# Kernel optimization log

Measured on AMD Instinct MI355X. Metric: run time of the kernel, lower is better.

The kernel has to match this reference:

```python
import jax, jax.numpy as jnp
import numpy as np

D_MODEL = 512
DK = 4
DV = 8
HIDD = 10
HEAD = D_MODEL // DV  # 64
LN_EPS = 1e-5


def setup_inputs() -> dict:
    key = jax.random.key(0)
    ks = jax.random.split(key, 10)
    B, S, Se = 8, 512, 512
    u = jax.random.uniform  # torch.rand initializer for attention weights
    n = jax.random.normal
    return {
        "x": n(ks[0], (B, S, D_MODEL), jnp.float32),
        "x_enc": n(ks[1], (B, Se, D_MODEL), jnp.float32),
        "WqM": u(ks[2], (D_MODEL, HEAD * DK), jnp.float32),
        "WkM": u(ks[3], (D_MODEL, HEAD * DK), jnp.float32),
        "WvM": u(ks[4], (D_MODEL, HEAD * DV), jnp.float32),
        "ln_g": jnp.ones((D_MODEL,), jnp.float32),
        "ln_b": jnp.zeros((D_MODEL,), jnp.float32),
        "fc1_w": n(ks[5], (HIDD, D_MODEL), jnp.float32) * (1.0 / np.sqrt(D_MODEL)),
        "fc1_b": jnp.zeros((HIDD,), jnp.float32),
        "fc2_w": n(ks[6], (D_MODEL, HIDD), jnp.float32) * (1.0 / np.sqrt(HIDD)),
        "fc2_b": jnp.zeros((D_MODEL,), jnp.float32),
    }


def _attention(Xq, Xkv, WqM, WkM, WvM, causal_mul_mask):
    # NOTE: cross-attention in the source also uses WqM/WkM/WvM (Wq/Wk/Wv unused).
    B, Sq, _ = Xq.shape
    Sk = Xkv.shape[1]
    Q = (Xq @ WqM).reshape(B, Sq, HEAD, DK)
    K = (Xkv @ WkM).reshape(B, Sk, HEAD, DK)
    V = (Xkv @ WvM).reshape(B, Sk, HEAD, DV)
    score = jnp.einsum('bqhd,bkhd->bhqk', Q, K) / np.sqrt(DK).astype(np.float32)
    if causal_mul_mask:
        # Faithful quirk: multiplicative tril mask on scores (NOT additive -inf).
        score = score * jnp.tril(jnp.ones((Sq, Sk), score.dtype))
    w = jax.nn.softmax(score, axis=-1)
    out = jnp.einsum('bhqk,bkhd->bqhd', w, V)
    return out.reshape(B, Sq, HEAD * DV)  # HEAD*DV == d_model


def _layernorm(x, g, b):
    mu = jnp.mean(x, axis=-1, keepdims=True)
    var = jnp.mean(jnp.square(x - mu), axis=-1, keepdims=True)
    return (x - mu) * jax.lax.rsqrt(var + LN_EPS) * g + b


def reference(x, x_enc, WqM, WkM, WvM, ln_g, ln_b, fc1_w, fc1_b, fc2_w, fc2_b):
    fx = _attention(x, x, WqM, WkM, WvM, causal_mul_mask=True)
    fx = _attention(fx, x_enc, WqM, WkM, WvM, causal_mul_mask=False)
    y = _layernorm(x + fx, ln_g, ln_b)
    h = jax.nn.relu(y @ fc1_w.T + fc1_b)
    return h @ fc2_w.T + fc2_b
```

## Files before the change

kernel.cpp:

```cpp
#include <hip/hip_runtime.h>
#include <math.h>

#define D_MODEL 512
#define BATCH 8
#define SEQ 512
#define HEAD 64
#define DK 4
#define DV 8
#define HIDD 10

#define MR 32
#define KC 32
#define NC 256

__global__ __launch_bounds__(256) void proj_kernel(
    const float* __restrict__ xq, const float* __restrict__ xkv,
    const float* __restrict__ Wq, const float* __restrict__ Wk,
    const float* __restrict__ Wv,
    float* __restrict__ Q2, float* __restrict__ K2, float* __restrict__ V2)
{
    __shared__ float xt[KC * MR];
    __shared__ float wt[KC * NC];

    const int t  = threadIdx.x;
    const int bj = blockIdx.x & 3;
    const int br = blockIdx.x >> 2;
    const int r0 = br * MR;

    const float* X; const float* W; int ldw; int c0;
    if (bj == 0)      { X = xq;  W = Wq; ldw = 256; c0 = 0;   }
    else if (bj == 1) { X = xkv; W = Wk; ldw = 256; c0 = 0;   }
    else if (bj == 2) { X = xkv; W = Wv; ldw = 512; c0 = 0;   }
    else              { X = xkv; W = Wv; ldw = 512; c0 = 256; }

    const int rg = t >> 6;
    const int cq = t & 63;
    const int rs = t & 31;
    const int kq = t >> 5;

    float4 acc[8];
#pragma unroll
    for (int r = 0; r < 8; ++r) acc[r] = make_float4(0.f, 0.f, 0.f, 0.f);

    for (int kc = 0; kc < D_MODEL; kc += KC) {
        const float4 xa = *(const float4*)(X + (long)(r0 + rs) * D_MODEL + kc + kq * 4);
        xt[(kq * 4 + 0) * MR + rs] = xa.x;
        xt[(kq * 4 + 1) * MR + rs] = xa.y;
        xt[(kq * 4 + 2) * MR + rs] = xa.z;
        xt[(kq * 4 + 3) * MR + rs] = xa.w;

#pragma unroll
        for (int i = 0; i < 8; ++i) {
            const int row = i * 4 + rg;
            *(float4*)(wt + row * NC + cq * 4) =
                *(const float4*)(W + (long)(kc + row) * ldw + c0 + cq * 4);
        }
        __syncthreads();

#pragma unroll 4
        for (int k = 0; k < KC; ++k) {
            const float4 w4 = *(const float4*)(wt + k * NC + cq * 4);
            const float4 x0 = *(const float4*)(xt + k * MR + rg * 8);
            const float4 x1 = *(const float4*)(xt + k * MR + rg * 8 + 4);
            const float xr[8] = {x0.x, x0.y, x0.z, x0.w, x1.x, x1.y, x1.z, x1.w};
#pragma unroll
            for (int r = 0; r < 8; ++r) {
                acc[r].x = fmaf(xr[r], w4.x, acc[r].x);
                acc[r].y = fmaf(xr[r], w4.y, acc[r].y);
                acc[r].z = fmaf(xr[r], w4.z, acc[r].z);
                acc[r].w = fmaf(xr[r], w4.w, acc[r].w);
            }
        }
        __syncthreads();
    }

    const int b = r0 >> 9;
    const int sb = (r0 & 511) + rg * 8;
    if (bj <= 1) {
        float* dst = (bj == 0) ? Q2 : K2;
#pragma unroll
        for (int r = 0; r < 8; ++r)
            *(float4*)(dst + (((long)b * HEAD + cq) * SEQ + sb + r) * 4) = acc[r];
    } else {
        const int col = c0 + cq * 4;
        const int h = col >> 3;
        const int off = col & 7;
#pragma unroll
        for (int r = 0; r < 8; ++r)
            *(float4*)(V2 + (((long)b * HEAD + h) * SEQ + sb + r) * 8 + off) = acc[r];
    }
}

__global__ __launch_bounds__(256) void attn_kernel(
    const float* __restrict__ Q2, const float* __restrict__ K2,
    const float* __restrict__ V2, float* __restrict__ O, int causal)
{
    extern __shared__ float smem[];
    float* Kl = smem;
    float* Vl = smem + SEQ * DK;
    float* cs = Vl + SEQ * DV;

    const int t = threadIdx.x;
    const int bh = blockIdx.x >> 1;
    const int qhalf = blockIdx.x & 1;
    const int b = bh >> 6;
    const int h = bh & 63;

    const float4* Ks = (const float4*)(K2 + (long)bh * SEQ * DK);
    ((float4*)Kl)[t]       = Ks[t];
    ((float4*)Kl)[t + 256] = Ks[t + 256];
    const float4* Vs = (const float4*)(V2 + (long)bh * SEQ * DV);
#pragma unroll
    for (int i = 0; i < 4; ++i)
        ((float4*)Vl)[t + i * 256] = Vs[t + i * 256];
    __syncthreads();

    if (causal) {
        const int ch = t >> 3, d = t & 7;
        float s16 = 0.f;
#pragma unroll
        for (int i = 0; i < 16; ++i) s16 += Vl[(ch * 16 + i) * 8 + d];
        cs[ch * 8 + d] = s16;
        __syncthreads();
        if (t < 8) {
            cs[256 + t] = 0.f;
            float run = 0.f;
            for (int c2 = 31; c2 >= 0; --c2) {
                run += cs[c2 * 8 + t];
                cs[c2 * 8 + t] = run;
            }
        }
        __syncthreads();
    }

    const int q = qhalf * 256 + t;
    const float4 qv = *(const float4*)(Q2 + ((long)bh * SEQ + q) * 4);
    const float q0 = qv.x * 0.5f, q1 = qv.y * 0.5f;
    const float q2 = qv.z * 0.5f, q3 = qv.w * 0.5f;

    const int bound = causal ? q : (SEQ - 1);

    float m = -INFINITY, l = 0.f;
    float a0=0.f,a1=0.f,a2=0.f,a3=0.f,a4=0.f,a5=0.f,a6=0.f,a7=0.f;

    int s0 = 0;
    for (; s0 + 8 <= bound + 1; s0 += 8) {
        float sc[8];
#pragma unroll
        for (int i = 0; i < 8; ++i) {
            const float4 k4 = *(const float4*)(Kl + (s0 + i) * 4);
            sc[i] = fmaf(q0, k4.x, fmaf(q1, k4.y, fmaf(q2, k4.z, q3 * k4.w)));
        }
        float gm = fmaxf(fmaxf(fmaxf(sc[0], sc[1]), fmaxf(sc[2], sc[3])),
                         fmaxf(fmaxf(sc[4], sc[5]), fmaxf(sc[6], sc[7])));
        if (gm > m) {
            float scale = __expf(m - gm);
            l *= scale;
            a0*=scale; a1*=scale; a2*=scale; a3*=scale;
            a4*=scale; a5*=scale; a6*=scale; a7*=scale;
            m = gm;
        }
#pragma unroll
        for (int i = 0; i < 8; ++i) {
            float p = __expf(sc[i] - m);
            l += p;
            const float4 v0 = *(const float4*)(Vl + (s0 + i) * 8);
            const float4 v1 = *(const float4*)(Vl + (s0 + i) * 8 + 4);
            a0 = fmaf(p, v0.x, a0); a1 = fmaf(p, v0.y, a1);
            a2 = fmaf(p, v0.z, a2); a3 = fmaf(p, v0.w, a3);
            a4 = fmaf(p, v1.x, a4); a5 = fmaf(p, v1.y, a5);
            a6 = fmaf(p, v1.z, a6); a7 = fmaf(p, v1.w, a7);
        }
    }
    for (int s = s0; s <= bound; ++s) {
        const float4 k4 = *(const float4*)(Kl + s * 4);
        float sc = fmaf(q0, k4.x, fmaf(q1, k4.y, fmaf(q2, k4.z, q3 * k4.w)));
        if (sc > m) {
            float scale = __expf(m - sc);
            l *= scale;
            a0*=scale; a1*=scale; a2*=scale; a3*=scale;
            a4*=scale; a5*=scale; a6*=scale; a7*=scale;
            m = sc;
        }
        float p = __expf(sc - m);
        l += p;
        const float4 v0 = *(const float4*)(Vl + s * 8);
        const float4 v1 = *(const float4*)(Vl + s * 8 + 4);
        a0 = fmaf(p, v0.x, a0); a1 = fmaf(p, v0.y, a1);
        a2 = fmaf(p, v0.z, a2); a3 = fmaf(p, v0.w, a3);
        a4 = fmaf(p, v1.x, a4); a5 = fmaf(p, v1.y, a5);
        a6 = fmaf(p, v1.z, a6); a7 = fmaf(p, v1.w, a7);
    }

    if (causal && q < SEQ - 1) {
        float M = fmaxf(m, 0.f);
        float scale = __expf(m - M);
        float pm = __expf(-M);
        l = l * scale + pm * (float)(SEQ - 1 - q);
        int nq = q + 1;
        int cq2 = nq >> 4;
        float sv[8];
#pragma unroll
        for (int d = 0; d < 8; ++d) sv[d] = cs[(cq2 + 1) * 8 + d];
        for (int s = nq; s < (cq2 + 1) * 16; ++s) {
            const float4 v0 = *(const float4*)(Vl + s * 8);
            const float4 v1 = *(const float4*)(Vl + s * 8 + 4);
            sv[0]+=v0.x; sv[1]+=v0.y; sv[2]+=v0.z; sv[3]+=v0.w;
            sv[4]+=v1.x; sv[5]+=v1.y; sv[6]+=v1.z; sv[7]+=v1.w;
        }
        a0 = a0*scale + pm*sv[0]; a1 = a1*scale + pm*sv[1];
        a2 = a2*scale + pm*sv[2]; a3 = a3*scale + pm*sv[3];
        a4 = a4*scale + pm*sv[4]; a5 = a5*scale + pm*sv[5];
        a6 = a6*scale + pm*sv[6]; a7 = a7*scale + pm*sv[7];
    }

    float inv = 1.0f / l;
    const long obase = (long)b * SEQ * 512 + (long)q * 512 + h * DV;
    *(float4*)(O + obase)     = make_float4(a0*inv, a1*inv, a2*inv, a3*inv);
    *(float4*)(O + obase + 4) = make_float4(a4*inv, a5*inv, a6*inv, a7*inv);
}

__global__ __launch_bounds__(256) void ln_mlp_kernel(
    const float* __restrict__ x, const float* __restrict__ fx,
    const float* __restrict__ g, const float* __restrict__ beta,
    const float* __restrict__ w1, const float* __restrict__ b1,
    const float* __restrict__ w2, const float* __restrict__ b2,
    float* __restrict__ out)
{
    const int t = threadIdx.x;
    const int lane = t & 63;
    const int row = blockIdx.x * 4 + (t >> 6);
    const long base = (long)row * D_MODEL;
    const int e0 = lane * 8;

    const float4 xa = *(const float4*)(x + base + e0);
    const float4 xb = *(const float4*)(x + base + e0 + 4);
    const float4 fa = *(const float4*)(fx + base + e0);
    const float4 fb = *(const float4*)(fx + base + e0 + 4);
    float z[8] = {xa.x+fa.x, xa.y+fa.y, xa.z+fa.z, xa.w+fa.w,
                  xb.x+fb.x, xb.y+fb.y, xb.z+fb.z, xb.w+fb.w};

    float sum = 0.f;
#pragma unroll
    for (int j = 0; j < 8; ++j) sum += z[j];
#pragma unroll
    for (int o = 32; o > 0; o >>= 1) sum += __shfl_xor(sum, o);
    float mu = sum * (1.0f / 512.0f);

    float d[8], ss = 0.f;
#pragma unroll
    for (int j = 0; j < 8; ++j) { d[j] = z[j] - mu; ss += d[j] * d[j]; }
#pragma unroll
    for (int o = 32; o > 0; o >>= 1) ss += __shfl_xor(ss, o);
    float rs = rsqrtf(ss * (1.0f / 512.0f) + 1e-5f);

    const float4 ga = *(const float4*)(g + e0);
    const float4 gb = *(const float4*)(g + e0 + 4);
    const float4 ba = *(const float4*)(beta + e0);
    const float4 bb = *(const float4*)(beta + e0 + 4);
    const float gg[8] = {ga.x,ga.y,ga.z,ga.w,gb.x,gb.y,gb.z,gb.w};
    const float bt[8] = {ba.x,ba.y,ba.z,ba.w,bb.x,bb.y,bb.z,bb.w};
    float y[8];
#pragma unroll
    for (int j = 0; j < 8; ++j) y[j] = d[j] * rs * gg[j] + bt[j];

    float part[HIDD];
#pragma unroll
    for (int i = 0; i < HIDD; ++i) {
        const float4 wa = *(const float4*)(w1 + i * 512 + e0);
        const float4 wb = *(const float4*)(w1 + i * 512 + e0 + 4);
        part[i] = y[0]*wa.x + y[1]*wa.y + y[2]*wa.z + y[3]*wa.w
                + y[4]*wb.x + y[5]*wb.y + y[6]*wb.z + y[7]*wb.w;
    }
#pragma unroll
    for (int i = 0; i < HIDD; ++i)
#pragma unroll
        for (int o = 32; o > 0; o >>= 1) part[i] += __shfl_xor(part[i], o);

    float hv[HIDD];
#pragma unroll
    for (int i = 0; i < HIDD; ++i) hv[i] = fmaxf(part[i] + b1[i], 0.f);

    float o8[8];
#pragma unroll
    for (int j = 0; j < 8; ++j) o8[j] = b2[e0 + j];
#pragma unroll
    for (int i = 0; i < HIDD; ++i)
#pragma unroll
        for (int j = 0; j < 8; ++j)
            o8[j] = fmaf(hv[i], w2[(long)(e0 + j) * 10 + i], o8[j]);

    *(float4*)(out + base + e0)     = make_float4(o8[0], o8[1], o8[2], o8[3]);
    *(float4*)(out + base + e0 + 4) = make_float4(o8[4], o8[5], o8[6], o8[7]);
}

extern "C" void kernel_launch(void* const* d_in, const int* in_sizes, int n_in,
                              void* d_out, int out_size, void* d_ws, size_t ws_size,
                              hipStream_t stream) {
    (void)in_sizes; (void)n_in; (void)out_size; (void)ws_size;
    const float* x    = (const float*)d_in[0];
    const float* xenc = (const float*)d_in[1];
    const float* Wq   = (const float*)d_in[2];
    const float* Wk   = (const float*)d_in[3];
    const float* Wv   = (const float*)d_in[4];
    const float* ln_g = (const float*)d_in[5];
    const float* ln_b = (const float*)d_in[6];
    const float* w1   = (const float*)d_in[7];
    const float* b1   = (const float*)d_in[8];
    const float* w2   = (const float*)d_in[9];
    const float* b2   = (const float*)d_in[10];
    float* out = (float*)d_out;

    float* ws = (float*)d_ws;
    float* Q2 = ws;
    float* K2 = Q2 + 1048576;
    float* V2 = K2 + 1048576;
    float* A  = V2 + 2097152;

    const int nrows = BATCH * SEQ;
    const size_t lds_cross  = (size_t)(SEQ * DK + SEQ * DV) * 4;
    const size_t lds_causal = lds_cross + (size_t)(33 * DV) * 4;
    const int proj_grid = (nrows / MR) * 4;

    proj_kernel<<<dim3(proj_grid), 256, 0, stream>>>(x, x, Wq, Wk, Wv, Q2, K2, V2);
    attn_kernel<<<dim3(BATCH * HEAD * 2), 256, lds_causal, stream>>>(Q2, K2, V2, A, 1);

    proj_kernel<<<dim3(proj_grid), 256, 0, stream>>>(A, xenc, Wq, Wk, Wv, Q2, K2, V2);
    attn_kernel<<<dim3(BATCH * HEAD * 2), 256, lds_cross, stream>>>(Q2, K2, V2, A, 0);

    ln_mlp_kernel<<<dim3(nrows / 4), 256, 0, stream>>>(x, A, ln_g, ln_b,
                                                       w1, b1, w2, b2, out);
}
```

Measured before the change: 341.9 us.

## Hoist cross-attention K/V projection into first proj pass, split-K Q projection

The first projection kernel now also computes the cross-attention K and V from x_enc, giving 7 column-block jobs in one launch instead of recomputing them later. The second projection shrinks to a dedicated Q-only kernel that splits K into two halves with small tiles, writing two partial Q buffers that the attention kernel sums on load. Softmax exponentials switch to exp2 with log2(e) folded into the query scale. The aim is better GPU fill for the small Q projection and less work on the serial path, at the cost of more workspace and an extra Q read in attention.

```diff
diff --git a/kernel.cpp b/kernel.cpp
--- a/kernel.cpp
+++ b/kernel.cpp
@@ -13,25 +13,37 @@
 #define KC 32
 #define NC 256
 
+__device__ __forceinline__ float4 fma4(float s, float4 w, float4 a) {
+    a.x = fmaf(s, w.x, a.x); a.y = fmaf(s, w.y, a.y);
+    a.z = fmaf(s, w.z, a.z); a.w = fmaf(s, w.w, a.w);
+    return a;
+}
+
 __global__ __launch_bounds__(256) void proj_kernel(
-    const float* __restrict__ xq, const float* __restrict__ xkv,
+    const float* __restrict__ x, const float* __restrict__ xe,
     const float* __restrict__ Wq, const float* __restrict__ Wk,
     const float* __restrict__ Wv,
-    float* __restrict__ Q2, float* __restrict__ K2, float* __restrict__ V2)
+    float* __restrict__ Q2, float* __restrict__ K2, float* __restrict__ V2,
+    float* __restrict__ Kc, float* __restrict__ Vc)
 {
     __shared__ float xt[KC * MR];
     __shared__ float wt[KC * NC];
 
     const int t  = threadIdx.x;
-    const int bj = blockIdx.x & 3;
-    const int br = blockIdx.x >> 2;
+    const int bj = blockIdx.x >> 7;
+    const int br = blockIdx.x & 127;
     const int r0 = br * MR;
 
-    const float* X; const float* W; int ldw; int c0;
-    if (bj == 0)      { X = xq;  W = Wq; ldw = 256; c0 = 0;   }
-    else if (bj == 1) { X = xkv; W = Wk; ldw = 256; c0 = 0;   }
-    else if (bj == 2) { X = xkv; W = Wv; ldw = 512; c0 = 0;   }
-    else              { X = xkv; W = Wv; ldw = 512; c0 = 256; }
+    const float* X; const float* W; int ldw; int c0; float* dst; int vt;
+    switch (bj) {
+      case 0:  X = x;  W = Wq; ldw = 256; c0 = 0;   dst = Q2; vt = 0; break;
+      case 1:  X = x;  W = Wk; ldw = 256; c0 = 0;   dst = K2; vt = 0; break;
+      case 2:  X = x;  W = Wv; ldw = 512; c0 = 0;   dst = V2; vt = 1; break;
+      case 3:  X = x;  W = Wv; ldw = 512; c0 = 256; dst = V2; vt = 1; break;
+      case 4:  X = xe; W = Wk; ldw = 256; c0 = 0;   dst = Kc; vt = 0; break;
+      case 5:  X = xe; W = Wv; ldw = 512; c0 = 0;   dst = Vc; vt = 1; break;
+      default: X = xe; W = Wv; ldw = 512; c0 = 256; dst = Vc; vt = 1; break;
+    }
 
     const int rg = t >> 6;
     const int cq = t & 63;
@@ -62,22 +74,21 @@
             const float4 w4 = *(const float4*)(wt + k * NC + cq * 4);
             const float4 x0 = *(const float4*)(xt + k * MR + rg * 8);
             const float4 x1 = *(const float4*)(xt + k * MR + rg * 8 + 4);
-            const float xr[8] = {x0.x, x0.y, x0.z, x0.w, x1.x, x1.y, x1.z, x1.w};
-#pragma unroll
-            for (int r = 0; r < 8; ++r) {
-                acc[r].x = fmaf(xr[r], w4.x, acc[r].x);
-                acc[r].y = fmaf(xr[r], w4.y, acc[r].y);
-                acc[r].z = fmaf(xr[r], w4.z, acc[r].z);
-                acc[r].w = fmaf(xr[r], w4.w, acc[r].w);
-            }
+            acc[0] = fma4(x0.x, w4, acc[0]);
+            acc[1] = fma4(x0.y, w4, acc[1]);
+            acc[2] = fma4(x0.z, w4, acc[2]);
+            acc[3] = fma4(x0.w, w4, acc[3]);
+            acc[4] = fma4(x1.x, w4, acc[4]);
+            acc[5] = fma4(x1.y, w4, acc[5]);
+            acc[6] = fma4(x1.z, w4, acc[6]);
+            acc[7] = fma4(x1.w, w4, acc[7]);
         }
         __syncthreads();
     }
 
     const int b = r0 >> 9;
     const int sb = (r0 & 511) + rg * 8;
-    if (bj <= 1) {
-        float* dst = (bj == 0) ? Q2 : K2;
+    if (vt == 0) {
 #pragma unroll
         for (int r = 0; r < 8; ++r)
             *(float4*)(dst + (((long)b * HEAD + cq) * SEQ + sb + r) * 4) = acc[r];
@@ -87,13 +98,69 @@
         const int off = col & 7;
 #pragma unroll
         for (int r = 0; r < 8; ++r)
-            *(float4*)(V2 + (((long)b * HEAD + h) * SEQ + sb + r) * 8 + off) = acc[r];
-    }
+            *(float4*)(dst + (((long)b * HEAD + h) * SEQ + sb + r) * 8 + off) = acc[r];
+    }
+}
+
+__global__ __launch_bounds__(256, 8) void proj2_kernel(
+    const float* __restrict__ A, const float* __restrict__ Wq,
+    float* __restrict__ Qa, float* __restrict__ Qb)
+{
+    __shared__ float xt[KC * 32];
+    __shared__ float wt[KC * 64];
+
+    const int t  = threadIdx.x;
+    const int kh = blockIdx.x & 1;
+    const int bj = (blockIdx.x >> 1) & 3;
+    const int br = blockIdx.x >> 3;
+    const int r0 = br * 32;
+    const int c0 = bj * 64;
+    const int kb = kh * 256;
+    float* dst = kh ? Qb : Qa;
+
+    const int cq = t & 15;
+    const int rr = t >> 4;
+    const int rs = t & 31, kq = t >> 5;
+
+    float4 acc[2];
+    acc[0] = make_float4(0.f, 0.f, 0.f, 0.f);
+    acc[1] = acc[0];
+
+    for (int kc = 0; kc < 256; kc += KC) {
+        const float4 xa = *(const float4*)(A + (long)(r0 + rs) * D_MODEL + kb + kc + kq * 4);
+        xt[(kq * 4 + 0) * 32 + rs] = xa.x;
+        xt[(kq * 4 + 1) * 32 + rs] = xa.y;
+        xt[(kq * 4 + 2) * 32 + rs] = xa.z;
+        xt[(kq * 4 + 3) * 32 + rs] = xa.w;
+#pragma unroll
+        for (int i = 0; i < 2; ++i) {
+            const int row = i * 16 + (t >> 4);
+            *(float4*)(wt + row * 64 + (t & 15) * 4) =
+                *(const float4*)(Wq + (long)(kb + kc + row) * 256 + c0 + (t & 15) * 4);
+        }
+        __syncthreads();
+#pragma unroll 4
+        for (int k = 0; k < KC; ++k) {
+            const float4 w4 = *(const float4*)(wt + k * 64 + cq * 4);
+            const float2 x2 = *(const float2*)(xt + k * 32 + rr * 2);
+            acc[0] = fma4(x2.x, w4, acc[0]);
+            acc[1] = fma4(x2.y, w4, acc[1]);
+        }
+        __syncthreads();
+    }
+
+    const int b  = r0 >> 9;
+    const int sb = (r0 & 511) + rr * 2;
+    const int h  = (c0 >> 2) + cq;
+#pragma unroll
+    for (int r = 0; r < 2; ++r)
+        *(float4*)(dst + (((long)b * HEAD + h) * SEQ + sb + r) * 4) = acc[r];
 }
 
 __global__ __launch_bounds__(256) void attn_kernel(
-    const float* __restrict__ Q2, const float* __restrict__ K2,
-    const float* __restrict__ V2, float* __restrict__ O, int causal)
+    const float* __restrict__ Qa, const float* __restrict__ Qb,
+    const float* __restrict__ K2, const float* __restrict__ V2,
+    float* __restrict__ O, int causal)
 {
     extern __shared__ float smem[];
     float* Kl = smem;
@@ -134,9 +201,14 @@
     }
 
     const int q = qhalf * 256 + t;
-    const float4 qv = *(const float4*)(Q2 + ((long)bh * SEQ + q) * 4);
-    const float q0 = qv.x * 0.5f, q1 = qv.y * 0.5f;
-    const float q2 = qv.z * 0.5f, q3 = qv.w * 0.5f;
+    float4 qv = *(const float4*)(Qa + ((long)bh * SEQ + q) * 4);
+    if (Qb) {
+        const float4 qw = *(const float4*)(Qb + ((long)bh * SEQ + q) * 4);
+        qv.x += qw.x; qv.y += qw.y; qv.z += qw.z; qv.w += qw.w;
+    }
+    const float cf = 0.5f * 1.44269504088896340736f;
+    const float q0 = qv.x * cf, q1 = qv.y * cf;
+    const float q2 = qv.z * cf, q3 = qv.w * cf;
 
     const int bound = causal ? q : (SEQ - 1);
 
@@ -154,7 +226,7 @@
         float gm = fmaxf(fmaxf(fmaxf(sc[0], sc[1]), fmaxf(sc[2], sc[3])),
                          fmaxf(fmaxf(sc[4], sc[5]), fmaxf(sc[6], sc[7])));
         if (gm > m) {
-            float scale = __expf(m - gm);
+            float scale = __builtin_amdgcn_exp2f(m - gm);
             l *= scale;
             a0*=scale; a1*=scale; a2*=scale; a3*=scale;
             a4*=scale; a5*=scale; a6*=scale; a7*=scale;
@@ -162,7 +234,7 @@
         }
 #pragma unroll
         for (int i = 0; i < 8; ++i) {
-            float p = __expf(sc[i] - m);
+            float p = __builtin_amdgcn_exp2f(sc[i] - m);
             l += p;
             const float4 v0 = *(const float4*)(Vl + (s0 + i) * 8);
             const float4 v1 = *(const float4*)(Vl + (s0 + i) * 8 + 4);
@@ -176,13 +248,13 @@
         const float4 k4 = *(const float4*)(Kl + s * 4);
         float sc = fmaf(q0, k4.x, fmaf(q1, k4.y, fmaf(q2, k4.z, q3 * k4.w)));
         if (sc > m) {
-            float scale = __expf(m - sc);
+            float scale = __builtin_amdgcn_exp2f(m - sc);
             l *= scale;
             a0*=scale; a1*=scale; a2*=scale; a3*=scale;
             a4*=scale; a5*=scale; a6*=scale; a7*=scale;
             m = sc;
         }
-        float p = __expf(sc - m);
+        float p = __builtin_amdgcn_exp2f(sc - m);
         l += p;
         const float4 v0 = *(const float4*)(Vl + s * 8);
         const float4 v1 = *(const float4*)(Vl + s * 8 + 4);
@@ -194,8 +266,8 @@
 
     if (causal && q < SEQ - 1) {
         float M = fmaxf(m, 0.f);
-        float scale = __expf(m - M);
-        float pm = __expf(-M);
+        float scale = __builtin_amdgcn_exp2f(m - M);
+        float pm = __builtin_amdgcn_exp2f(-M);
         l = l * scale + pm * (float)(SEQ - 1 - q);
         int nq = q + 1;
         int cq2 = nq >> 4;
@@ -312,22 +384,25 @@
     float* out = (float*)d_out;
 
     float* ws = (float*)d_ws;
-    float* Q2 = ws;
-    float* K2 = Q2 + 1048576;
-    float* V2 = K2 + 1048576;
-    float* A  = V2 + 2097152;
-
-    const int nrows = BATCH * SEQ;
+    float* Q1 = ws;
+    float* K1 = ws +  1048576;
+    float* V1 = ws +  2097152;
+    float* Kc = ws +  4194304;
+    float* Vc = ws +  5242880;
+    float* A  = ws +  7340032;
+    float* Qa = ws +  9437184;
+    float* Qb = ws + 10485760;
+
     const size_t lds_cross  = (size_t)(SEQ * DK + SEQ * DV) * 4;
     const size_t lds_causal = lds_cross + (size_t)(33 * DV) * 4;
-    const int proj_grid = (nrows / MR) * 4;
-
-    proj_kernel<<<dim3(proj_grid), 256, 0, stream>>>(x, x, Wq, Wk, Wv, Q2, K2, V2);
-    attn_kernel<<<dim3(BATCH * HEAD * 2), 256, lds_causal, stream>>>(Q2, K2, V2, A, 1);
-
-    proj_kernel<<<dim3(proj_grid), 256, 0, stream>>>(A, xenc, Wq, Wk, Wv, Q2, K2, V2);
-    attn_kernel<<<dim3(BATCH * HEAD * 2), 256, lds_cross, stream>>>(Q2, K2, V2, A, 0);
-
-    ln_mlp_kernel<<<dim3(nrows / 4), 256, 0, stream>>>(x, A, ln_g, ln_b,
-                                                       w1, b1, w2, b2, out);
-}
+
+    proj_kernel<<<dim3(896), 256, 0, stream>>>(x, xenc, Wq, Wk, Wv,
+                                               Q1, K1, V1, Kc, Vc);
+    attn_kernel<<<dim3(BATCH * HEAD * 2), 256, lds_causal, stream>>>(
+        Q1, nullptr, K1, V1, A, 1);
+    proj2_kernel<<<dim3(1024), 256, 0, stream>>>(A, Wq, Qa, Qb);
+    attn_kernel<<<dim3(BATCH * HEAD * 2), 256, lds_cross, stream>>>(
+        Qa, Qb, Kc, Vc, A, 0);
+    ln_mlp_kernel<<<dim3(1024), 256, 0, stream>>>(x, A, ln_g, ln_b,
+                                                  w1, b1, w2, b2, out);
+}
```

Measured after the change: 343.3 us. About the same (+0.4%).
